# Kernel optimization log

Measured on AMD Instinct MI355X. Metric: run time of the kernel, lower is better.

Reference implementation:

```python
import jax, jax.numpy as jnp
import numpy as np

B, T, V, E, H = 64, 512, 8192, 1024, 2048


def setup_inputs() -> dict:
    key = jax.random.key(0)
    k = jax.random.split(key, 8)
    idx = jax.random.randint(k[0], (B, T), 0, V)
    targets = jax.random.randint(k[1], (B, T), 0, V)
    s = 0.02
    W_E = jax.random.normal(k[2], (V, E), jnp.float32) * s
    start = jnp.zeros((1, H), jnp.float32)
    W_xh = jax.random.normal(k[3], (E + H, H), jnp.float32) * s  # Linear(E+H -> H)
    b_xh = jnp.zeros((H,), jnp.float32)
    W_head = jax.random.normal(k[4], (H, V), jnp.float32) * s
    b_head = jnp.zeros((V,), jnp.float32)
    return {"idx": idx, "targets": targets, "W_E": W_E, "start": start,
            "W_xh": W_xh, "b_xh": b_xh, "W_head": W_head, "b_head": b_head}


def reference(idx, targets, W_E, start, W_xh, b_xh, W_head, b_head):
    b, t = idx.shape
    emb = W_E[idx]  # [B, T, E]
    # split concat-linear: cat([x,h]) @ W_xh == x @ Wx + h @ Wh (same math)
    Wx, Wh = W_xh[:E], W_xh[E:]
    xproj = jnp.einsum('bte,eh->bth', emb, Wx) + b_xh  # precompute input part

    def step(h_prev, xp_t):
        h_t = jnp.tanh(xp_t + h_prev @ Wh)
        return h_t, h_t

    h0 = jnp.broadcast_to(start, (b, H))
    _, hs = jax.lax.scan(step, h0, jnp.swapaxes(xproj, 0, 1))  # [T, B, H]
    hidden = jnp.swapaxes(hs, 0, 1)  # [B, T, H]
    logits = jnp.einsum('bth,hv->btv', hidden, W_head) + b_head

    # cross entropy with ignore_index=-1
    logp = jax.nn.log_softmax(logits, axis=-1)
    mask = targets != -1
    tsafe = jnp.where(mask, targets, 0)
    nll = -jnp.take_along_axis(logp, tsafe[..., None], axis=-1)[..., 0]
    loss = jnp.sum(nll * mask) / jnp.maximum(jnp.sum(mask), 1)
    return logits, loss
```

## Files before the change

### kernel.cpp

```cpp
#include <hip/hip_runtime.h>
#include <hip/hip_bf16.h>
#include <math.h>
#include <stdint.h>

#define Bb 64
#define Tt 512
#define Vv 8192
#define Ee 1024
#define Hh 2048

typedef unsigned short u16;
typedef unsigned long long u64;
typedef __attribute__((ext_vector_type(8))) short bf16x8;
typedef __attribute__((ext_vector_type(8))) _Float16 f16x8;
typedef __attribute__((ext_vector_type(4))) float f32x4;

__device__ __forceinline__ u16 f2b(float f) {
  unsigned u = __float_as_uint(f);
  u += 0x7FFF + ((u >> 16) & 1);
  return (u16)(u >> 16);
}
__device__ __forceinline__ float b2f(u16 h) {
  return __uint_as_float(((unsigned)h) << 16);
}
__device__ __forceinline__ u16 f2h_bits(float f) {
  union { _Float16 h; u16 u; } c;
  c.h = (_Float16)f;
  return c.u;
}

__device__ __forceinline__ void gload16f(f16x8& dst, const void* addr) {
  asm volatile("global_load_dwordx4 %0, %1, off sc1"
               : "=v"(dst) : "v"(addr) : "memory");
}
__device__ __forceinline__ void gstore2_sc1(void* addr, unsigned val) {
  asm volatile("global_store_short %0, %1, off sc1"
               :: "v"(addr), "v"(val) : "memory");
}

__device__ __forceinline__ void gll16(const u16* g, const u16* l) {
  __builtin_amdgcn_global_load_lds((__attribute__((address_space(1))) void*)g,
                                   (__attribute__((address_space(3))) void*)l, 16, 0, 0);
}

__device__ __forceinline__ float wave_max(float v) {
  #pragma unroll
  for (int d = 32; d; d >>= 1) v = fmaxf(v, __shfl_xor(v, d, 64));
  return v;
}
__device__ __forceinline__ float wave_sum(float v) {
  #pragma unroll
  for (int d = 32; d; d >>= 1) v += __shfl_xor(v, d, 64);
  return v;
}


__global__ __launch_bounds__(256)
void embed_cast_f16(const float* __restrict__ WE, const int* __restrict__ idx,
                    u16* __restrict__ emb) {
  const int m = blockIdx.x;
  const int row = idx[m];
  const float4 v = ((const float4*)(WE + (size_t)row * Ee))[threadIdx.x];
  ushort4 o;
  o.x = f2h_bits(v.x); o.y = f2h_bits(v.y);
  o.z = f2h_bits(v.z); o.w = f2h_bits(v.w);
  ((ushort4*)(emb + (size_t)m * Ee))[threadIdx.x] = o;
}

__global__ __launch_bounds__(256)
void transpose_cast_f16(const float* __restrict__ src, u16* __restrict__ dst,
                        int R, int C) {
  __shared__ float tile[32][33];
  const int bi = blockIdx.x;
  const int bj = blockIdx.y;
  const int tid = threadIdx.x;
  const int r  = tid >> 3;
  const int c4 = (tid & 7) * 4;
  float4 v = *(const float4*)(src + (size_t)(bj * 32 + r) * C + bi * 32 + c4);
  tile[r][c4 + 0] = v.x; tile[r][c4 + 1] = v.y;
  tile[r][c4 + 2] = v.z; tile[r][c4 + 3] = v.w;
  __syncthreads();
  ushort4 o;
  o.x = f2h_bits(tile[c4 + 0][r]); o.y = f2h_bits(tile[c4 + 1][r]);
  o.z = f2h_bits(tile[c4 + 2][r]); o.w = f2h_bits(tile[c4 + 3][r]);
  *(ushort4*)(dst + (size_t)(bi * 32 + r) * R + bj * 32 + c4) = o;
}

__global__ __launch_bounds__(256)
void h0_init(const float* __restrict__ start, u16* __restrict__ hbuf) {
  const int b = blockIdx.x;
  #pragma unroll
  for (int j = 0; j < 8; ++j) {
    int n = threadIdx.x * 8 + j;
    hbuf[(size_t)b * 2048 + n] = f2h_bits(start[n]);
  }
}

template <int MODE, int F16>
__global__ __launch_bounds__(512, 2)
void gemm256(const u16* __restrict__ A, const u16* __restrict__ Bt,
             const float* __restrict__ bias, void* __restrict__ outp,
             float* __restrict__ pm, float* __restrict__ ps,
             int M, int N, int K) {
  __shared__ u16 lds[65536];

  const int tid = threadIdx.x;
  const int lane = tid & 63;
  const int w = tid >> 6;
  const int wm = w >> 2;
  const int wn = w & 3;
  const int l15 = lane & 15, l16 = lane >> 4;

  const int nwg = gridDim.x * gridDim.y;
  const int lin = blockIdx.y * gridDim.x + blockIdx.x;
  const int swz = (lin & 7) * (nwg >> 3) + (lin >> 3);
  const int bm = swz % gridDim.x;
  const int bn = swz / gridDim.x;
  const int bm256 = bm * 256, bn256 = bn * 256;

  const size_t srcLane = (size_t)l15 * K + l16 * 8;
  #define STG(P, R0, kt, base)                                                 \
    {                                                                          \
      gll16((P) + (size_t)((R0) + w * 16) * K + (size_t)(kt) * 32 + srcLane,   \
            &lds[(base) + w * 512]);                                           \
      gll16((P) + (size_t)((R0) + (8 + w) * 16) * K + (size_t)(kt) * 32 + srcLane, \
            &lds[(base) + (8 + w) * 512]);                                     \
    }
  #define DSF(base, rbase) \
    (*(const bf16x8*)&lds[(base) + ((rbase) >> 4) * 512 + l16 * 128 + l15 * 8])
  #define MM1(a, b, c)                                                          \
    (F16 ? __builtin_amdgcn_mfma_f32_16x16x32_f16(*(const f16x8*)&(a),          \
                                                  *(const f16x8*)&(b), (c), 0, 0, 0) \
         : __builtin_amdgcn_mfma_f32_16x16x32_bf16((a), (b), (c), 0, 0, 0))

  f32x4 acc[8][4];
  #pragma unroll
  for (int m = 0; m < 8; ++m)
    #pragma unroll
    for (int n = 0; n < 4; ++n)
      acc[m][n] = (f32x4){0.f, 0.f, 0.f, 0.f};

  const int NT = K >> 5;

  for (int pt = 0; pt < 3; ++pt) {
    STG(A,  bm256, pt, pt * 8192);
    STG(Bt, bn256, pt, 32768 + pt * 8192);
  }
  asm volatile("s_waitcnt vmcnt(0)" ::: "memory");
  __builtin_amdgcn_s_barrier();

  for (int t = 0; t < NT; ++t) {
    const int abase = (t & 3) * 8192;
    const int bbase = 32768 + (t & 3) * 8192;
    const int sb = (t + 3) & 3;
    const bool stg = (t + 3 < NT);
    bf16x8 aR[4], bR[4];

    #pragma unroll
    for (int j = 0; j < 4; ++j) bR[j] = DSF(bbase, wn * 64 + j * 16);
    #pragma unroll
    for (int i = 0; i < 4; ++i) aR[i] = DSF(abase, wm * 128 + i * 16);
    if (stg) {
      STG(A, bm256, t + 3, sb * 8192);
      asm volatile("s_waitcnt vmcnt(8)" ::: "memory");
    } else {
      asm volatile("s_waitcnt vmcnt(0)" ::: "memory");
    }
    __builtin_amdgcn_s_barrier();
    asm volatile("s_waitcnt lgkmcnt(0)" ::: "memory");
    __builtin_amdgcn_sched_barrier(0);
    __builtin_amdgcn_s_setprio(1);
    #pragma unroll
    for (int i = 0; i < 4; ++i)
      #pragma unroll
      for (int j = 0; j < 4; ++j)
        acc[i][j] = MM1(aR[i], bR[j], acc[i][j]);
    __builtin_amdgcn_s_setprio(0);
    __builtin_amdgcn_s_barrier();

    #pragma unroll
    for (int i = 0; i < 4; ++i) aR[i] = DSF(abase, wm * 128 + 64 + i * 16);
    if (stg) {
      STG(Bt, bn256, t + 3, 32768 + sb * 8192);
      asm volatile("s_waitcnt vmcnt(8)" ::: "memory");
    } else {
      asm volatile("s_waitcnt vmcnt(0)" ::: "memory");
    }
    __builtin_amdgcn_s_barrier();
    asm volatile("s_waitcnt lgkmcnt(0)" ::: "memory");
    __builtin_amdgcn_sched_barrier(0);
    __builtin_amdgcn_s_setprio(1);
    #pragma unroll
    for (int i = 0; i < 4; ++i)
      #pragma unroll
      for (int j = 0; j < 4; ++j)
        acc[4 + i][j] = MM1(aR[i], bR[j], acc[4 + i][j]);
    __builtin_amdgcn_s_setprio(0);
    __builtin_amdgcn_s_barrier();
  }

  const int c0 = bn256 + wn * 64 + l15;
  float bv[4];
  #pragma unroll
  for (int j = 0; j < 4; ++j) bv[j] = bias[c0 + j * 16];

  if (MODE == 0) {
    float* scr = (float*)lds;
    float* outf = (float*)outp;
    #pragma unroll
    for (int fm = 0; fm < 8; ++fm) {
      #pragma unroll
      for (int q = 0; q < 4; ++q) {
        const int rl = wm * 128 + (fm >> 2) * 64 + (fm & 3) * 16 + l16 * 4 + q;
        const int row = bm256 + rl;
        float v0 = acc[fm][0][q] + bv[0];
        float v1 = acc[fm][1][q] + bv[1];
        float v2 = acc[fm][2][q] + bv[2];
        float v3 = acc[fm][3][q] + bv[3];
        outf[(size_t)row * N + c0]      = v0;
        outf[(size_t)row * N + c0 + 16] = v1;
        outf[(size_t)row * N + c0 + 32] = v2;
        outf[(size_t)row * N + c0 + 48] = v3;
        float mx = fmaxf(fmaxf(v0, v1), fmaxf(v2, v3));
        #pragma unroll
        for (int d = 1; d < 16; d <<= 1) mx = fmaxf(mx, __shfl_xor(mx, d, 64));
        float se = expf(v0 - mx) + expf(v1 - mx) + expf(v2 - mx) + expf(v3 - mx);
        #pragma unroll
        for (int d = 1; d < 16; d <<= 1) se += __shfl_xor(se, d, 64);
        if (l15 == 0) {
          scr[wn * 256 + rl] = mx;
          scr[1024 + wn * 256 + rl] = se;
        }
      }
    }
    __syncthreads();
    if (lane < 32) {
      const int rl = w * 32 + lane;
      float m0 = scr[rl], m1 = scr[256 + rl], m2 = scr[512 + rl], m3 = scr[768 + rl];
      float Mx = fmaxf(fmaxf(m0, m1), fmaxf(m2, m3));
      float S = scr[1024 + rl] * expf(m0 - Mx) + scr[1280 + rl] * expf(m1 - Mx)
              + scr[1536 + rl] * expf(m2 - Mx) + scr[1792 + rl] * expf(m3 - Mx);
      const int row = bm256 + rl;
      const int nbn = N >> 8;
      pm[(size_t)row * nbn + bn] = Mx;
      ps[(size_t)row * nbn + bn] = S;
    }
  } else {
    u16* outh = (u16*)outp;
    #pragma unroll
    for (int fm = 0; fm < 8; ++fm) {
      #pragma unroll
      for (int q = 0; q < 4; ++q) {
        const int row = bm256 + wm * 128 + (fm >> 2) * 64 + (fm & 3) * 16 + l16 * 4 + q;
        const int b = row >> 9, t = row & 511;
        u16* dst = outh + ((size_t)t * Bb + b) * N + c0;
        dst[0]  = f2b(acc[fm][0][q] + bv[0]);
        dst[16] = f2b(acc[fm][1][q] + bv[1]);
        dst[32] = f2b(acc[fm][2][q] + bv[2]);
        dst[48] = f2b(acc[fm][3][q] + bv[3]);
      }
    }
  }
  #undef STG
  #undef DSF
  #undef MM1
}

__global__ __launch_bounds__(512, 2)
void rnn_scan(const u16* __restrict__ WhT, const u16* __restrict__ xp,
              u16* __restrict__ hbuf, u16* __restrict__ hidden,
              unsigned* __restrict__ sync) {
  __shared__ u16 whi[65536];
  __shared__ float red[4096];

  const int bid = blockIdx.x;
  const int g = bid >> 6;
  const int colg = bid & 63;
  const int rowbase = g * 16;
  const int col0 = colg * 32;
  const int tid = threadIdx.x;
  const int lane = tid & 63;
  const int w = tid >> 6;

  for (int i = tid; i < 8192; i += 512) {
    const int ch = i & 3;
    const int cl = (i >> 2) & 15;
    const int kt = (i >> 6) & 63;
    const int c2 = (i >> 12) & 1;
    bf16x8 v = *(const bf16x8*)(WhT + (size_t)(col0 + c2 * 16 + cl) * 2048 + kt * 32 + ch * 8);
    *(bf16x8*)&whi[(size_t)(c2 * 64 + kt) * 512 + ch * 128 + cl * 8] = v;
  }
  __syncthreads();

  unsigned* cnt = sync + g * 64;
  bool dead = false;
  const int hrow = rowbase + (lane & 15);

  const int ev = w * 64 + lane;
  const int ef = ev >> 8;
  const int ep = ev & 255;
  const int el = ep >> 2, eq = ep & 3;
  const int erow = rowbase + (el & 15);
  const int ecol = col0 + ef * 16 + ((el >> 4) << 2) + eq;

  u16 xv16 = xp[(size_t)erow * 2048 + ecol];

  for (int t = 0; t < Tt; ++t) {
    const u16* hp = hbuf + (size_t)(t & 1) * (64 * 2048);
    u16*       hn = hbuf + (size_t)((t + 1) & 1) * (64 * 2048);

    f16x8 qh[8];
    const u16* hb = hp + (size_t)hrow * 2048 + (lane >> 4) * 8;
    #pragma unroll
    for (int kt = 0; kt < 8; ++kt)
      gload16f(qh[kt], hb + (w * 8 + kt) * 32);
    asm volatile("s_waitcnt vmcnt(0)" ::: "memory");
    __builtin_amdgcn_sched_barrier(0);

    f32x4 a0 = (f32x4){0.f, 0.f, 0.f, 0.f};
    f32x4 a1 = (f32x4){0.f, 0.f, 0.f, 0.f};
    #pragma unroll
    for (int kt = 0; kt < 8; ++kt) {
      const int ktG = w * 8 + kt;
      f16x8 w0 = *(const f16x8*)&whi[(size_t)(0 * 64 + ktG) * 512 + (lane >> 4) * 128 + (lane & 15) * 8];
      f16x8 w1 = *(const f16x8*)&whi[(size_t)(1 * 64 + ktG) * 512 + (lane >> 4) * 128 + (lane & 15) * 8];
      a0 = __builtin_amdgcn_mfma_f32_16x16x32_f16(w0, qh[kt], a0, 0, 0, 0);
      a1 = __builtin_amdgcn_mfma_f32_16x16x32_f16(w1, qh[kt], a1, 0, 0, 0);
    }

    *(f32x4*)&red[(w) * 256 + lane * 4]     = a0;
    *(f32x4*)&red[(8 + w) * 256 + lane * 4] = a1;
    __syncthreads();

    {
      float s = 0.f;
      #pragma unroll
      for (int j = 0; j < 8; ++j)
        s += red[(ef * 8 + j) * 256 + ep];
      float hv = tanhf(s + b2f(xv16));
      u16 hf = f2h_bits(hv);
      gstore2_sc1(hn + (size_t)erow * 2048 + ecol, (unsigned)hf);
      hidden[((size_t)erow * Tt + t) * Hh + ecol] = hf;
    }

    __syncthreads();
    if (t + 1 < Tt)
      xv16 = xp[((size_t)(t + 1) * Bb + erow) * 2048 + ecol];
    if (tid == 0) {
      unsigned old = __hip_atomic_fetch_add(cnt, 1u, __ATOMIC_RELAXED, __HIP_MEMORY_SCOPE_AGENT);
      if (old != (unsigned)(t * 64 + 63) && !dead) {
        unsigned polls = 0;
        while (__hip_atomic_load(cnt, __ATOMIC_RELAXED, __HIP_MEMORY_SCOPE_AGENT)
               < (unsigned)((t + 1) * 64)) {
          __builtin_amdgcn_s_sleep(1);
          if (++polls > 1000000u) { dead = true; break; }
        }
      }
    }
    __syncthreads();
  }
}


__global__ __launch_bounds__(256)
void nll_from_partials(const float* __restrict__ pm, const float* __restrict__ ps,
                       const float* __restrict__ logits, const int* __restrict__ tgt,
                       float* __restrict__ nll) {
  const int r = blockIdx.x * 4 + (threadIdx.x >> 6);
  const int lane = threadIdx.x & 63;
  float m = (lane < 32) ? pm[(size_t)r * 32 + lane] : -1e30f;
  float s = (lane < 32) ? ps[(size_t)r * 32 + lane] : 0.f;
  float M = wave_max(m);
  float S = wave_sum(s * expf(m - M));
  if (lane == 0) {
    const int tg = tgt[r];
    float o = 0.f;
    if (tg != -1) o = M + logf(S) - logits[(size_t)r * Vv + tg];
    nll[r] = o;
  }
}

__global__ __launch_bounds__(256)
void loss_reduce(const float* __restrict__ nll, const int* __restrict__ tgt,
                 float* __restrict__ out) {
  const int tid = threadIdx.x;
  float s = 0.f, c = 0.f;
  for (int i = tid; i < Bb * Tt; i += 256) {
    s += nll[i];
    c += (tgt[i] != -1) ? 1.f : 0.f;
  }
  s = wave_sum(s);
  c = wave_sum(c);
  __shared__ float as_[4], ac_[4];
  const int w = tid >> 6;
  if ((tid & 63) == 0) { as_[w] = s; ac_[w] = c; }
  __syncthreads();
  if (tid == 0) {
    float S = as_[0] + as_[1] + as_[2] + as_[3];
    float C = ac_[0] + ac_[1] + ac_[2] + ac_[3];
    out[0] = S / fmaxf(C, 1.f);
  }
}


extern "C" void kernel_launch(void* const* d_in, const int* in_sizes, int n_in,
                              void* d_out, int out_size, void* d_ws, size_t ws_size,
                              hipStream_t stream) {
  const int*   idx    = (const int*)d_in[0];
  const int*   tgt    = (const int*)d_in[1];
  const float* W_E    = (const float*)d_in[2];
  const float* start  = (const float*)d_in[3];
  const float* W_xh   = (const float*)d_in[4];
  const float* b_xh   = (const float*)d_in[5];
  const float* W_head = (const float*)d_in[6];
  const float* b_head = (const float*)d_in[7];

  char* ws = (char*)d_ws;
  u16*      emb16  = (u16*)(ws);
  u16*      hidden = (u16*)(ws);
  u16*      xproj  = (u16*)(ws + (size_t)128 * 1024 * 1024);
  float*    pm     = (float*)(ws + (size_t)128 * 1024 * 1024);
  float*    ps     = (float*)(ws + (size_t)136 * 1024 * 1024);
  u16*      WheadT = (u16*)(ws + (size_t)256 * 1024 * 1024);
  u16*      WhT    = (u16*)(ws + (size_t)288 * 1024 * 1024);
  u16*      WxT16  = (u16*)(ws + (size_t)304 * 1024 * 1024);
  u16*      hbuf   = (u16*)(ws + (size_t)312 * 1024 * 1024);
  float*    nll    = (float*)(ws + (size_t)313 * 1024 * 1024);
  unsigned* sync   = (unsigned*)(ws + (size_t)313 * 1024 * 1024 + 128 * 1024);

  embed_cast_f16<<<Bb * Tt, 256, 0, stream>>>(W_E, idx, emb16);
  transpose_cast_f16<<<dim3(Hh / 32, Ee / 32), 256, 0, stream>>>(W_xh, WxT16, Ee, Hh);
  transpose_cast_f16<<<dim3(Hh / 32, Hh / 32), 256, 0, stream>>>(W_xh + (size_t)Ee * Hh, WhT, Hh, Hh);
  transpose_cast_f16<<<dim3(Vv / 32, Hh / 32), 256, 0, stream>>>(W_head, WheadT, Hh, Vv);
  h0_init<<<Bb, 256, 0, stream>>>(start, hbuf);
  hipMemsetAsync(sync, 0, 1024, stream);

  gemm256<1, 1><<<dim3(128, 8), 512, 0, stream>>>(emb16, WxT16, b_xh, xproj, nullptr, nullptr,
                                                  Bb * Tt, Hh, 1024);

  rnn_scan<<<256, 512, 0, stream>>>(WhT, xproj, hbuf, hidden, sync);

  gemm256<0, 1><<<dim3(128, 32), 512, 0, stream>>>(hidden, WheadT, b_head, d_out, pm, ps,
                                                   Bb * Tt, Vv, 2048);

  nll_from_partials<<<Bb * Tt / 4, 256, 0, stream>>>(pm, ps, (const float*)d_out, tgt, nll);
  loss_reduce<<<1, 256, 0, stream>>>(nll, tgt, (float*)d_out + ((size_t)out_size - 1));
}
```

Measured before the change: 4.172 ms.

## Fuse prep kernels into one launch and deepen GEMM LDS pipeline to five stages

Merges the embedding gather, three transpose-casts, h0 init and the sync memset into a single prep_all kernel, removing several launches and the inter-kernel gaps between them. Separately, the GEMM grows its LDS ring from four to five buffers (160KB), prefetches four tiles ahead and relaxes the vmcnt waits to keep more loads in flight. The larger LDS footprint may stop two blocks fitting per CU, which would reduce occupancy for both GEMMs.

```diff
diff --git a/kernel.cpp b/kernel.cpp
--- a/kernel.cpp
+++ b/kernel.cpp
@@ -55,25 +55,10 @@
 }
 
 
-__global__ __launch_bounds__(256)
-void embed_cast_f16(const float* __restrict__ WE, const int* __restrict__ idx,
-                    u16* __restrict__ emb) {
-  const int m = blockIdx.x;
-  const int row = idx[m];
-  const float4 v = ((const float4*)(WE + (size_t)row * Ee))[threadIdx.x];
-  ushort4 o;
-  o.x = f2h_bits(v.x); o.y = f2h_bits(v.y);
-  o.z = f2h_bits(v.z); o.w = f2h_bits(v.w);
-  ((ushort4*)(emb + (size_t)m * Ee))[threadIdx.x] = o;
-}
-
-__global__ __launch_bounds__(256)
-void transpose_cast_f16(const float* __restrict__ src, u16* __restrict__ dst,
-                        int R, int C) {
-  __shared__ float tile[32][33];
-  const int bi = blockIdx.x;
-  const int bj = blockIdx.y;
-  const int tid = threadIdx.x;
+__device__ __forceinline__ void tr_cast_f16(const float* __restrict__ src,
+                                            u16* __restrict__ dst, int R, int C,
+                                            int bi, int bj, int tid,
+                                            float (*tile)[33]) {
   const int r  = tid >> 3;
   const int c4 = (tid & 7) * 4;
   float4 v = *(const float4*)(src + (size_t)(bj * 32 + r) * C + bi * 32 + c4);
@@ -87,12 +72,40 @@
 }
 
 __global__ __launch_bounds__(256)
-void h0_init(const float* __restrict__ start, u16* __restrict__ hbuf) {
+void prep_all(const float* __restrict__ WE, const int* __restrict__ idx,
+              u16* __restrict__ emb,
+              const float* __restrict__ W_xh, u16* __restrict__ WxT16,
+              u16* __restrict__ WhT,
+              const float* __restrict__ W_head, u16* __restrict__ WheadT,
+              const float* __restrict__ start, u16* __restrict__ hbuf,
+              unsigned* __restrict__ sync) {
+  __shared__ float tile[32][33];
   const int b = blockIdx.x;
-  #pragma unroll
-  for (int j = 0; j < 8; ++j) {
-    int n = threadIdx.x * 8 + j;
-    hbuf[(size_t)b * 2048 + n] = f2h_bits(start[n]);
+  const int tid = threadIdx.x;
+  if (b < 32768) {
+    const int row = idx[b];
+    const float4 v = ((const float4*)(WE + (size_t)row * Ee))[tid];
+    ushort4 o;
+    o.x = f2h_bits(v.x); o.y = f2h_bits(v.y);
+    o.z = f2h_bits(v.z); o.w = f2h_bits(v.w);
+    ((ushort4*)(emb + (size_t)b * Ee))[tid] = o;
+  } else if (b < 34816) {
+    const int s = b - 32768;
+    tr_cast_f16(W_xh, WxT16, Ee, Hh, s % 64, s / 64, tid, tile);
+  } else if (b < 38912) {
+    const int s = b - 34816;
+    tr_cast_f16(W_xh + (size_t)Ee * Hh, WhT, Hh, Hh, s % 64, s / 64, tid, tile);
+  } else if (b < 55296) {
+    const int s = b - 38912;
+    tr_cast_f16(W_head, WheadT, Hh, Vv, s % 256, s / 256, tid, tile);
+  } else {
+    const int s = b - 55296;
+    #pragma unroll
+    for (int j = 0; j < 8; ++j) {
+      int n = tid * 8 + j;
+      hbuf[(size_t)s * 2048 + n] = f2h_bits(start[n]);
+    }
+    if (s == 0) sync[tid] = 0;
   }
 }
 
@@ -102,7 +115,7 @@
              const float* __restrict__ bias, void* __restrict__ outp,
              float* __restrict__ pm, float* __restrict__ ps,
              int M, int N, int K) {
-  __shared__ u16 lds[65536];
+  __shared__ u16 lds[81920];
 
   const int tid = threadIdx.x;
   const int lane = tid & 63;
@@ -126,6 +139,8 @@
       gll16((P) + (size_t)((R0) + (8 + w) * 16) * K + (size_t)(kt) * 32 + srcLane, \
             &lds[(base) + (8 + w) * 512]);                                     \
     }
+  #define ABUF(t) (((t) % 5) * 8192)
+  #define BBUF(t) (40960 + ((t) % 5) * 8192)
   #define DSF(base, rbase) \
     (*(const bf16x8*)&lds[(base) + ((rbase) >> 4) * 512 + l16 * 128 + l15 * 8])
   #define MM1(a, b, c)                                                          \
@@ -142,18 +157,17 @@
 
   const int NT = K >> 5;
 
-  for (int pt = 0; pt < 3; ++pt) {
-    STG(A,  bm256, pt, pt * 8192);
-    STG(Bt, bn256, pt, 32768 + pt * 8192);
+  for (int pt = 0; pt < 4; ++pt) {
+    STG(A,  bm256, pt, ABUF(pt));
+    STG(Bt, bn256, pt, BBUF(pt));
   }
   asm volatile("s_waitcnt vmcnt(0)" ::: "memory");
   __builtin_amdgcn_s_barrier();
 
   for (int t = 0; t < NT; ++t) {
-    const int abase = (t & 3) * 8192;
-    const int bbase = 32768 + (t & 3) * 8192;
-    const int sb = (t + 3) & 3;
-    const bool stg = (t + 3 < NT);
+    const int abase = ABUF(t);
+    const int bbase = BBUF(t);
+    const bool stg = (t + 4 < NT);
     bf16x8 aR[4], bR[4];
 
     #pragma unroll
@@ -161,8 +175,8 @@
     #pragma unroll
     for (int i = 0; i < 4; ++i) aR[i] = DSF(abase, wm * 128 + i * 16);
     if (stg) {
-      STG(A, bm256, t + 3, sb * 8192);
-      asm volatile("s_waitcnt vmcnt(8)" ::: "memory");
+      STG(A, bm256, t + 4, ABUF(t + 4));
+      asm volatile("s_waitcnt vmcnt(14)" ::: "memory");
     } else {
       asm volatile("s_waitcnt vmcnt(0)" ::: "memory");
     }
@@ -181,8 +195,8 @@
     #pragma unroll
     for (int i = 0; i < 4; ++i) aR[i] = DSF(abase, wm * 128 + 64 + i * 16);
     if (stg) {
-      STG(Bt, bn256, t + 3, 32768 + sb * 8192);
-      asm volatile("s_waitcnt vmcnt(8)" ::: "memory");
+      STG(Bt, bn256, t + 4, BBUF(t + 4));
+      asm volatile("s_waitcnt vmcnt(14)" ::: "memory");
     } else {
       asm volatile("s_waitcnt vmcnt(0)" ::: "memory");
     }
@@ -262,6 +276,8 @@
     }
   }
   #undef STG
+  #undef ABUF
+  #undef BBUF
   #undef DSF
   #undef MM1
 }
@@ -428,12 +444,8 @@
   float*    nll    = (float*)(ws + (size_t)313 * 1024 * 1024);
   unsigned* sync   = (unsigned*)(ws + (size_t)313 * 1024 * 1024 + 128 * 1024);
 
-  embed_cast_f16<<<Bb * Tt, 256, 0, stream>>>(W_E, idx, emb16);
-  transpose_cast_f16<<<dim3(Hh / 32, Ee / 32), 256, 0, stream>>>(W_xh, WxT16, Ee, Hh);
-  transpose_cast_f16<<<dim3(Hh / 32, Hh / 32), 256, 0, stream>>>(W_xh + (size_t)Ee * Hh, WhT, Hh, Hh);
-  transpose_cast_f16<<<dim3(Vv / 32, Hh / 32), 256, 0, stream>>>(W_head, WheadT, Hh, Vv);
-  h0_init<<<Bb, 256, 0, stream>>>(start, hbuf);
-  hipMemsetAsync(sync, 0, 1024, stream);
+  prep_all<<<55360, 256, 0, stream>>>(W_E, idx, emb16, W_xh, WxT16, WhT,
+                                      W_head, WheadT, start, hbuf, sync);
 
   gemm256<1, 1><<<dim3(128, 8), 512, 0, stream>>>(emb16, WxT16, b_xh, xproj, nullptr, nullptr,
                                                   Bb * Tt, Hh, 1024);
```

After: 4.195 ms. Within noise of the previous version (+0.5%).
